# Optimization experiments

Hardware: AMD Instinct MI355X
Metric: run time of the kernel (lower is better)

## Reference

```python
import jax, jax.numpy as jnp
import numpy as np

N, E, D, L = 50000, 600000, 128, 2  # nodes, edges, hidden_dim, num_gnn_layers
NEG_SLOPE = 0.2  # PyG GATv2Conv default negative_slope


def setup_inputs() -> dict:
    key = jax.random.key(0)
    ks = jax.random.split(key, 10)
    s = 1.0 / np.sqrt(D)
    return {
        "x": jax.random.normal(ks[0], (N, D), jnp.float32),
        "edge_index": jax.random.randint(ks[1], (2, E), 0, N, dtype=jnp.int32),
        # per-layer GATv2 params (stacked over L layers)
        "Wl": jax.random.normal(ks[2], (L, D, D), jnp.float32) * s,  # lin_l (source)
        "bl": jnp.zeros((L, D), jnp.float32),
        "Wr": jax.random.normal(ks[3], (L, D, D), jnp.float32) * s,  # lin_r (target)
        "br": jnp.zeros((L, D), jnp.float32),
        "att": jax.random.normal(ks[4], (L, D), jnp.float32) * s,
        "bias": jnp.zeros((L, D), jnp.float32),
        # shared residual Linear
        "W_res": jax.random.normal(ks[5], (D, D), jnp.float32) * s,
        "b_res": jnp.zeros((D,), jnp.float32),
    }


def reference(x, edge_index, Wl, bl, Wr, br, att, bias, W_res, b_res):
    n = x.shape[0]
    # add self loops (PyG GATv2Conv default add_self_loops=True)
    loops = jnp.arange(n, dtype=edge_index.dtype)
    src = jnp.concatenate([edge_index[0], loops])  # source j (messages)
    dst = jnp.concatenate([edge_index[1], loops])  # target i (aggregation)

    def conv(h, i):
        xl = h @ Wl[i] + bl[i]  # [N, D] source transform
        xr = h @ Wr[i] + br[i]  # [N, D] target transform
        m = xl[src] + xr[dst]   # [E+N, D] gathered edge messages
        e = jnp.einsum('ed,d->e', jnp.where(m > 0, m, NEG_SLOPE * m), att[i])
        # segment softmax over incoming edges of each destination node
        emax = jax.lax.stop_gradient(jax.ops.segment_max(e, dst, num_segments=n))
        ex = jnp.exp(e - emax[dst])
        denom = jax.ops.segment_sum(ex, dst, num_segments=n)
        alpha = ex / (denom[dst] + 1e-16)
        out = jax.ops.segment_sum(alpha[:, None] * xl[src], dst, num_segments=n)
        return out + bias[i]

    for i in range(Wl.shape[0]):
        x = jax.nn.relu(conv(x, i) + x @ W_res + b_res)
    return x
```

## Files before the change

### kernel.cpp

```cpp
#include <hip/hip_runtime.h>
#include <math.h>


#define DIM 128
#define NEG_SLOPE 0.2f
#define TPW 4

typedef __attribute__((ext_vector_type(8))) short short8;
typedef __attribute__((ext_vector_type(4))) float floatx4;

static __device__ __forceinline__ unsigned short f2b(float f) {
    unsigned u = __float_as_uint(f);
    unsigned r = (u + 0x7FFFu + ((u >> 16) & 1u)) >> 16;
    return (unsigned short)r;
}
static __device__ __forceinline__ float b2f(unsigned short h) {
    return __uint_as_float(((unsigned)h) << 16);
}

__global__ void k_init_counts(int* __restrict__ counts, int n) {
    int i = blockIdx.x * blockDim.x + threadIdx.x;
    if (i < n) counts[i] = 1;
}

__global__ void k_count(const int* __restrict__ dst, int E, int* __restrict__ counts) {
    int k = blockIdx.x * blockDim.x + threadIdx.x;
    if (k < E) atomicAdd(&counts[dst[k]], 1);
}

__global__ void k_scan1(const int* __restrict__ counts, int n,
                        int* __restrict__ rowptr, int* __restrict__ bsum) {
    __shared__ int s[256];
    int tid = threadIdx.x;
    int i = blockIdx.x * 256 + tid;
    int v = (i < n) ? counts[i] : 0;
    s[tid] = v;
    __syncthreads();
    for (int off = 1; off < 256; off <<= 1) {
        int t = (tid >= off) ? s[tid - off] : 0;
        __syncthreads();
        s[tid] += t;
        __syncthreads();
    }
    if (i < n) rowptr[i + 1] = s[tid];
    if (tid == 255) bsum[blockIdx.x] = s[255];
}

__global__ void k_scan2(int* __restrict__ bsum, int nb) {
    __shared__ int s[256];
    int tid = threadIdx.x;
    int v = (tid < nb) ? bsum[tid] : 0;
    s[tid] = v;
    __syncthreads();
    for (int off = 1; off < 256; off <<= 1) {
        int t = (tid >= off) ? s[tid - off] : 0;
        __syncthreads();
        s[tid] += t;
        __syncthreads();
    }
    if (tid < nb) bsum[tid] = s[tid];
}

__global__ void k_scan3(int* __restrict__ rowptr, const int* __restrict__ bsum,
                        int n, int* __restrict__ counts_to_cursors) {
    int i = blockIdx.x * 256 + threadIdx.x;
    if (i < n) {
        int add = (blockIdx.x > 0) ? bsum[blockIdx.x - 1] : 0;
        int cnt = counts_to_cursors[i];
        int v = rowptr[i + 1] + add;
        rowptr[i + 1] = v;
        counts_to_cursors[i] = v - cnt;
    }
    if (i == 0) rowptr[0] = 0;
}

__global__ void k_scatter(const int* __restrict__ src, const int* __restrict__ dst,
                          int E, int n, int* __restrict__ cur, int* __restrict__ srt) {
    int k = blockIdx.x * blockDim.x + threadIdx.x;
    int tot = E + n;
    if (k >= tot) return;
    int s, d;
    if (k < E) { s = src[k]; d = dst[k]; }
    else       { s = k - E;  d = s; }
    int p = atomicAdd(&cur[d], 1);
    srt[p] = s;
}

__global__ void k_wfrag(const float* __restrict__ Wl, const float* __restrict__ Wr,
                        const float* __restrict__ Wres, unsigned short* __restrict__ out) {
    int idx = blockIdx.x * blockDim.x + threadIdx.x;
    if (idx >= 2 * 3 * 4 * 8 * 64) return;
    int lane = idx & 63;
    int nr   = (idx >> 6) & 7;
    int ks   = (idx >> 9) & 3;
    int v    = idx >> 11;
    int sec = v % 3, l = v / 3;
    const float* W = (sec == 0) ? (Wl + l * DIM * DIM)
                   : (sec == 1) ? (Wr + l * DIM * DIM) : Wres;
    int nn = nr * 16 + (lane & 15);
    int k0 = ks * 32 + ((lane >> 4) << 3);
    ushort4 a, b;
    a.x = f2b(W[(k0 + 0) * DIM + nn]); a.y = f2b(W[(k0 + 1) * DIM + nn]);
    a.z = f2b(W[(k0 + 2) * DIM + nn]); a.w = f2b(W[(k0 + 3) * DIM + nn]);
    b.x = f2b(W[(k0 + 4) * DIM + nn]); b.y = f2b(W[(k0 + 5) * DIM + nn]);
    b.z = f2b(W[(k0 + 6) * DIM + nn]); b.w = f2b(W[(k0 + 7) * DIM + nn]);
    *(ushort4*)(out + (size_t)idx * 8) = a;
    *(ushort4*)(out + (size_t)idx * 8 + 4) = b;
}

__global__ void k_hfrag(const float* __restrict__ h, unsigned short* __restrict__ out,
                        int n, int ntiles) {
    int idx = blockIdx.x * blockDim.x + threadIdx.x;
    if (idx >= ntiles * 256) return;
    int lane = idx & 63;
    int ks   = (idx >> 6) & 3;
    int tile = idx >> 8;
    int row  = tile * 16 + (lane & 15);
    int col0 = ks * 32 + ((lane >> 4) << 3);
    ushort4 a = {0, 0, 0, 0}, b = {0, 0, 0, 0};
    if (row < n) {
        float4 v0 = *(const float4*)(h + (size_t)row * DIM + col0);
        float4 v1 = *(const float4*)(h + (size_t)row * DIM + col0 + 4);
        a.x = f2b(v0.x); a.y = f2b(v0.y); a.z = f2b(v0.z); a.w = f2b(v0.w);
        b.x = f2b(v1.x); b.y = f2b(v1.y); b.z = f2b(v1.z); b.w = f2b(v1.w);
    }
    *(ushort4*)(out + (size_t)idx * 8) = a;
    *(ushort4*)(out + (size_t)idx * 8 + 4) = b;
}

__global__ __launch_bounds__(256, 2) void k_gemm(
    const unsigned short* __restrict__ hfrag, const unsigned short* __restrict__ wfrag,
    const float* __restrict__ bl, const float* __restrict__ br, const float* __restrict__ bres,
    unsigned short* __restrict__ XLb, float* __restrict__ XR, float* __restrict__ RES,
    int ntiles)
{
    int sec  = blockIdx.y;
    int lane = threadIdx.x & 63;
    int w    = threadIdx.x >> 6;

    const unsigned short* wbase = wfrag + (size_t)sec * (4 * 8 * 64 * 8);
    short8 bf[4][8];
#pragma unroll
    for (int ks = 0; ks < 4; ks++)
#pragma unroll
        for (int nr = 0; nr < 8; nr++)
            bf[ks][nr] = *(const short8*)(wbase + (((ks * 8 + nr) * 64 + lane) << 3));

    const float* bias = (sec == 0) ? bl : (sec == 1) ? br : bres;
    int colb = (lane >> 4) << 2;
    float4 bv[8];
#pragma unroll
    for (int nr = 0; nr < 8; nr++) bv[nr] = *(const float4*)(bias + nr * 16 + colb);

    int wid = blockIdx.x * 4 + w;
#pragma unroll
    for (int i = 0; i < TPW; i++) {
        int t = wid * TPW + i;
        if (t >= ntiles) break;
        short8 a[4];
#pragma unroll
        for (int ks = 0; ks < 4; ks++)
            a[ks] = *(const short8*)(hfrag + (((t * 4 + ks) * 64 + lane) << 3));
        floatx4 acc[8];
#pragma unroll
        for (int nr = 0; nr < 8; nr++) acc[nr] = (floatx4){0.f, 0.f, 0.f, 0.f};
#pragma unroll
        for (int ks = 0; ks < 4; ks++)
#pragma unroll
            for (int nr = 0; nr < 8; nr++)
                acc[nr] = __builtin_amdgcn_mfma_f32_16x16x32_bf16(bf[ks][nr], a[ks], acc[nr], 0, 0, 0);

        int row = t * 16 + (lane & 15);
        size_t rb = (size_t)row * DIM;
#pragma unroll
        for (int nr = 0; nr < 8; nr++) {
            float4 o;
            o.x = acc[nr][0] + bv[nr].x;
            o.y = acc[nr][1] + bv[nr].y;
            o.z = acc[nr][2] + bv[nr].z;
            o.w = acc[nr][3] + bv[nr].w;
            int col = nr * 16 + colb;
            if (sec == 0) {
                ushort4 u;
                u.x = f2b(o.x); u.y = f2b(o.y); u.z = f2b(o.z); u.w = f2b(o.w);
                *(ushort4*)(XLb + rb + col) = u;
            } else if (sec == 1) {
                *(float4*)(XR + rb + col) = o;
            } else {
                *(float4*)(RES + rb + col) = o;
            }
        }
    }
}

__global__ __launch_bounds__(256) void k_aggr(
    const unsigned short* __restrict__ XLb, const float* __restrict__ XR,
    const float* __restrict__ RES, const float* __restrict__ att,
    const float* __restrict__ bias, const int* __restrict__ rowptr,
    const int* __restrict__ srt, float* __restrict__ outF,
    unsigned short* __restrict__ fragOut, int writeFrag, int n)
{
    int wave = threadIdx.x >> 6;
    int lane = threadIdx.x & 63;
    int node = blockIdx.x * 4 + wave;
    if (node >= n) return;
    int half = lane >> 5, sl = lane & 31;
    int d0 = sl << 2;

    float4 a4 = *(const float4*)(att + d0);
    float4 x4 = *(const float4*)(XR + (size_t)node * DIM + d0);
    int beg = rowptr[node], end = rowptr[node + 1];
    int len = end - beg;
    int hl = (len + 1) >> 1;
    int sb = beg + half * hl;
    int se = half ? end : (beg + hl);

    float m = -INFINITY, den = 0.f;
    float ax = 0.f, ay = 0.f, az = 0.f, aw = 0.f;

    int j = sb;
    for (; j + 4 <= se; j += 4) {
        int s0 = srt[j], s1 = srt[j + 1], s2 = srt[j + 2], s3 = srt[j + 3];
        ushort4 u0 = *(const ushort4*)(XLb + (size_t)s0 * DIM + d0);
        ushort4 u1 = *(const ushort4*)(XLb + (size_t)s1 * DIM + d0);
        ushort4 u2 = *(const ushort4*)(XLb + (size_t)s2 * DIM + d0);
        ushort4 u3 = *(const ushort4*)(XLb + (size_t)s3 * DIM + d0);
        float v0x = b2f(u0.x), v0y = b2f(u0.y), v0z = b2f(u0.z), v0w = b2f(u0.w);
        float v1x = b2f(u1.x), v1y = b2f(u1.y), v1z = b2f(u1.z), v1w = b2f(u1.w);
        float v2x = b2f(u2.x), v2y = b2f(u2.y), v2z = b2f(u2.z), v2w = b2f(u2.w);
        float v3x = b2f(u3.x), v3y = b2f(u3.y), v3z = b2f(u3.z), v3w = b2f(u3.w);
        float t, p0, p1, p2, p3;
        t = v0x + x4.x; p0  = fmaxf(t, NEG_SLOPE * t) * a4.x;
        t = v0y + x4.y; p0 += fmaxf(t, NEG_SLOPE * t) * a4.y;
        t = v0z + x4.z; p0 += fmaxf(t, NEG_SLOPE * t) * a4.z;
        t = v0w + x4.w; p0 += fmaxf(t, NEG_SLOPE * t) * a4.w;
        t = v1x + x4.x; p1  = fmaxf(t, NEG_SLOPE * t) * a4.x;
        t = v1y + x4.y; p1 += fmaxf(t, NEG_SLOPE * t) * a4.y;
        t = v1z + x4.z; p1 += fmaxf(t, NEG_SLOPE * t) * a4.z;
        t = v1w + x4.w; p1 += fmaxf(t, NEG_SLOPE * t) * a4.w;
        t = v2x + x4.x; p2  = fmaxf(t, NEG_SLOPE * t) * a4.x;
        t = v2y + x4.y; p2 += fmaxf(t, NEG_SLOPE * t) * a4.y;
        t = v2z + x4.z; p2 += fmaxf(t, NEG_SLOPE * t) * a4.z;
        t = v2w + x4.w; p2 += fmaxf(t, NEG_SLOPE * t) * a4.w;
        t = v3x + x4.x; p3  = fmaxf(t, NEG_SLOPE * t) * a4.x;
        t = v3y + x4.y; p3 += fmaxf(t, NEG_SLOPE * t) * a4.y;
        t = v3z + x4.z; p3 += fmaxf(t, NEG_SLOPE * t) * a4.z;
        t = v3w + x4.w; p3 += fmaxf(t, NEG_SLOPE * t) * a4.w;
#pragma unroll
        for (int off = 16; off >= 1; off >>= 1) {
            p0 += __shfl_xor(p0, off);
            p1 += __shfl_xor(p1, off);
            p2 += __shfl_xor(p2, off);
            p3 += __shfl_xor(p3, off);
        }
        float pm = fmaxf(fmaxf(p0, p1), fmaxf(p2, p3));
        float mn = fmaxf(m, pm);
        float c  = __expf(m - mn);
        float w0 = __expf(p0 - mn), w1 = __expf(p1 - mn);
        float w2 = __expf(p2 - mn), w3 = __expf(p3 - mn);
        ax = ax * c + w0 * v0x + w1 * v1x + w2 * v2x + w3 * v3x;
        ay = ay * c + w0 * v0y + w1 * v1y + w2 * v2y + w3 * v3y;
        az = az * c + w0 * v0z + w1 * v1z + w2 * v2z + w3 * v3z;
        aw = aw * c + w0 * v0w + w1 * v1w + w2 * v2w + w3 * v3w;
        den = den * c + w0 + w1 + w2 + w3;
        m = mn;
    }
    for (; j < se; j++) {
        int s0 = srt[j];
        ushort4 u0 = *(const ushort4*)(XLb + (size_t)s0 * DIM + d0);
        float v0x = b2f(u0.x), v0y = b2f(u0.y), v0z = b2f(u0.z), v0w = b2f(u0.w);
        float t, p0;
        t = v0x + x4.x; p0  = fmaxf(t, NEG_SLOPE * t) * a4.x;
        t = v0y + x4.y; p0 += fmaxf(t, NEG_SLOPE * t) * a4.y;
        t = v0z + x4.z; p0 += fmaxf(t, NEG_SLOPE * t) * a4.z;
        t = v0w + x4.w; p0 += fmaxf(t, NEG_SLOPE * t) * a4.w;
#pragma unroll
        for (int off = 16; off >= 1; off >>= 1) p0 += __shfl_xor(p0, off);
        float mn = fmaxf(m, p0);
        float c  = __expf(m - mn);
        float w0 = __expf(p0 - mn);
        ax = ax * c + w0 * v0x;
        ay = ay * c + w0 * v0y;
        az = az * c + w0 * v0z;
        aw = aw * c + w0 * v0w;
        den = den * c + w0;
        m = mn;
    }

    float om   = __shfl_xor(m, 32);
    float oden = __shfl_xor(den, 32);
    float ox = __shfl_xor(ax, 32), oy = __shfl_xor(ay, 32);
    float oz = __shfl_xor(az, 32), ow = __shfl_xor(aw, 32);
    float M  = fmaxf(m, om);
    float se_ = __expf(m - M), so = __expf(om - M);
    float D  = den * se_ + oden * so + 1e-16f;
    float inv = 1.f / D;

    float4 r4 = *(const float4*)(RES + (size_t)node * DIM + d0);
    float4 b4 = *(const float4*)(bias + d0);
    float4 o;
    o.x = fmaxf((ax * se_ + ox * so) * inv + b4.x + r4.x, 0.f);
    o.y = fmaxf((ay * se_ + oy * so) * inv + b4.y + r4.y, 0.f);
    o.z = fmaxf((az * se_ + oz * so) * inv + b4.z + r4.z, 0.f);
    o.w = fmaxf((aw * se_ + ow * so) * inv + b4.w + r4.w, 0.f);

    if (half == 0) {
        if (writeFrag) {
            int tile = node >> 4;
            int ks = sl >> 3;
            int li = (node & 15) + (((sl >> 1) & 3) << 4);
            int j0 = (sl & 1) << 2;
            ushort4 u;
            u.x = f2b(o.x); u.y = f2b(o.y); u.z = f2b(o.z); u.w = f2b(o.w);
            *(ushort4*)(fragOut + ((size_t)((tile * 4 + ks) * 64 + li) << 3) + j0) = u;
        } else {
            *(float4*)(outF + (size_t)node * DIM + d0) = o;
        }
    }
}

extern "C" void kernel_launch(void* const* d_in, const int* in_sizes, int n_in,
                              void* d_out, int out_size, void* d_ws, size_t ws_size,
                              hipStream_t stream) {
    const float* x    = (const float*)d_in[0];
    const int*   ei   = (const int*)d_in[1];
    const float* Wl   = (const float*)d_in[2];
    const float* bl   = (const float*)d_in[3];
    const float* Wr   = (const float*)d_in[4];
    const float* br   = (const float*)d_in[5];
    const float* att  = (const float*)d_in[6];
    const float* bias = (const float*)d_in[7];
    const float* Wres = (const float*)d_in[8];
    const float* bres = (const float*)d_in[9];

    int n = in_sizes[0] / DIM;
    int E = in_sizes[1] / 2;
    int ntiles = (n + 15) >> 4;
    const int* srcIdx = ei;
    const int* dstIdx = ei + E;

    float* xr   = (float*)d_ws;
    float* resb = xr + (size_t)n * DIM;
    unsigned short* xlb   = (unsigned short*)(resb + (size_t)n * DIM);
    unsigned short* hfrag = xlb + (size_t)n * DIM;
    unsigned short* wfrag = hfrag + (size_t)ntiles * 16 * DIM;
    int* rowptr = (int*)(wfrag + 2 * 3 * DIM * DIM);
    int* tmpc   = rowptr + (n + 1);
    int* srt    = tmpc + n;
    int* bsum   = srt + (E + n);

    int nb1 = (n + 255) / 256;

    k_init_counts<<<(n + 255) / 256, 256, 0, stream>>>(tmpc, n);
    k_count<<<(E + 255) / 256, 256, 0, stream>>>(dstIdx, E, tmpc);
    k_scan1<<<nb1, 256, 0, stream>>>(tmpc, n, rowptr, bsum);
    k_scan2<<<1, 256, 0, stream>>>(bsum, nb1);
    k_scan3<<<nb1, 256, 0, stream>>>(rowptr, bsum, n, tmpc);
    k_scatter<<<(E + n + 255) / 256, 256, 0, stream>>>(srcIdx, dstIdx, E, n, tmpc, srt);
    k_wfrag<<<(2 * 3 * 4 * 8 * 64 + 255) / 256, 256, 0, stream>>>(Wl, Wr, Wres, wfrag);
    k_hfrag<<<(ntiles * 256 + 255) / 256, 256, 0, stream>>>(x, hfrag, n, ntiles);

    int gx = (ntiles + 4 * TPW - 1) / (4 * TPW);
    for (int l = 0; l < 2; l++) {
        dim3 g(gx, 3);
        k_gemm<<<g, 256, 0, stream>>>(hfrag, wfrag + (size_t)l * 3 * 4 * 8 * 64 * 8,
                                      bl + (size_t)l * DIM, br + (size_t)l * DIM, bres,
                                      xlb, xr, resb, ntiles);
        k_aggr<<<(n + 3) / 4, 256, 0, stream>>>(xlb, xr, resb, att + (size_t)l * DIM,
                                                bias + (size_t)l * DIM, rowptr, srt,
                                                (float*)d_out, hfrag, (l == 0) ? 1 : 0, n);
    }
}
```

Before: 218.7 us.

## Merge preprocessing kernels, single-block scan, bf16 XR, 8-way packed aggregation

Replaces the three-kernel scan with a single 1024-thread block scan, zero-initialises counts with a memset, and fuses weight and feature fragment conversion into one launch. XR is stored as bf16 to halve its traffic. The aggregation loop processes 8 edges per iteration using packed f32 ops and a rewritten leaky-ReLU (0.6t+0.4|t|), with masked tails. Risks include unaligned int4 index loads, over-reads past segment ends, and extra bf16 rounding of XR.

New measurement: 354.7 us. 62.2% more time.

```diff
diff --git a/kernel.cpp b/kernel.cpp
--- a/kernel.cpp
+++ b/kernel.cpp
@@ -8,6 +8,7 @@
 
 typedef __attribute__((ext_vector_type(8))) short short8;
 typedef __attribute__((ext_vector_type(4))) float floatx4;
+typedef __attribute__((ext_vector_type(2))) float f32x2;
 
 static __device__ __forceinline__ unsigned short f2b(float f) {
     unsigned u = __float_as_uint(f);
@@ -17,10 +18,32 @@
 static __device__ __forceinline__ float b2f(unsigned short h) {
     return __uint_as_float(((unsigned)h) << 16);
 }
-
-__global__ void k_init_counts(int* __restrict__ counts, int n) {
-    int i = blockIdx.x * blockDim.x + threadIdx.x;
-    if (i < n) counts[i] = 1;
+static __device__ __forceinline__ f32x2 cvt2(unsigned u) {
+    f32x2 r;
+    r.x = __uint_as_float(u << 16);
+    r.y = __uint_as_float(u & 0xffff0000u);
+    return r;
+}
+static __device__ __forceinline__ f32x2 pk_add(f32x2 a, f32x2 b) {
+    f32x2 d;
+    asm("v_pk_add_f32 %0, %1, %2" : "=v"(d) : "v"(a), "v"(b));
+    return d;
+}
+static __device__ __forceinline__ f32x2 pk_mul(f32x2 a, f32x2 b) {
+    f32x2 d;
+    asm("v_pk_mul_f32 %0, %1, %2" : "=v"(d) : "v"(a), "v"(b));
+    return d;
+}
+static __device__ __forceinline__ f32x2 pk_fma(f32x2 a, f32x2 b, f32x2 c) {
+    f32x2 d;
+    asm("v_pk_fma_f32 %0, %1, %2, %3" : "=v"(d) : "v"(a), "v"(b), "v"(c));
+    return d;
+}
+static __device__ __forceinline__ f32x2 pk_abs2(f32x2 a) {
+    f32x2 r;
+    r.x = __builtin_fabsf(a.x);
+    r.y = __builtin_fabsf(a.y);
+    return r;
 }
 
 __global__ void k_count(const int* __restrict__ dst, int E, int* __restrict__ counts) {
@@ -28,50 +51,31 @@
     if (k < E) atomicAdd(&counts[dst[k]], 1);
 }
 
-__global__ void k_scan1(const int* __restrict__ counts, int n,
-                        int* __restrict__ rowptr, int* __restrict__ bsum) {
-    __shared__ int s[256];
+__global__ __launch_bounds__(1024) void k_scan(int* __restrict__ cnt, int n,
+                                               int* __restrict__ rowptr) {
+    __shared__ int sh[1024];
     int tid = threadIdx.x;
-    int i = blockIdx.x * 256 + tid;
-    int v = (i < n) ? counts[i] : 0;
-    s[tid] = v;
+    int chunk = (n + 1023) >> 10;
+    int b = tid * chunk;
+    int e = min(b + chunk, n);
+    int s = 0;
+    for (int i = b; i < e; i++) s += cnt[i] + 1;
+    sh[tid] = s;
     __syncthreads();
-    for (int off = 1; off < 256; off <<= 1) {
-        int t = (tid >= off) ? s[tid - off] : 0;
+    for (int off = 1; off < 1024; off <<= 1) {
+        int t = (tid >= off) ? sh[tid - off] : 0;
         __syncthreads();
-        s[tid] += t;
+        sh[tid] += t;
         __syncthreads();
     }
-    if (i < n) rowptr[i + 1] = s[tid];
-    if (tid == 255) bsum[blockIdx.x] = s[255];
-}
-
-__global__ void k_scan2(int* __restrict__ bsum, int nb) {
-    __shared__ int s[256];
-    int tid = threadIdx.x;
-    int v = (tid < nb) ? bsum[tid] : 0;
-    s[tid] = v;
-    __syncthreads();
-    for (int off = 1; off < 256; off <<= 1) {
-        int t = (tid >= off) ? s[tid - off] : 0;
-        __syncthreads();
-        s[tid] += t;
-        __syncthreads();
-    }
-    if (tid < nb) bsum[tid] = s[tid];
-}
-
-__global__ void k_scan3(int* __restrict__ rowptr, const int* __restrict__ bsum,
-                        int n, int* __restrict__ counts_to_cursors) {
-    int i = blockIdx.x * 256 + threadIdx.x;
-    if (i < n) {
-        int add = (blockIdx.x > 0) ? bsum[blockIdx.x - 1] : 0;
-        int cnt = counts_to_cursors[i];
-        int v = rowptr[i + 1] + add;
-        rowptr[i + 1] = v;
-        counts_to_cursors[i] = v - cnt;
-    }
-    if (i == 0) rowptr[0] = 0;
+    int run = sh[tid] - s;
+    for (int i = b; i < e; i++) {
+        int c = cnt[i] + 1;
+        cnt[i] = run;
+        run += c;
+        rowptr[i + 1] = run;
+    }
+    if (tid == 0) rowptr[0] = 0;
 }
 
 __global__ void k_scatter(const int* __restrict__ src, const int* __restrict__ dst,
@@ -86,53 +90,54 @@
     srt[p] = s;
 }
 
-__global__ void k_wfrag(const float* __restrict__ Wl, const float* __restrict__ Wr,
-                        const float* __restrict__ Wres, unsigned short* __restrict__ out) {
-    int idx = blockIdx.x * blockDim.x + threadIdx.x;
-    if (idx >= 2 * 3 * 4 * 8 * 64) return;
-    int lane = idx & 63;
-    int nr   = (idx >> 6) & 7;
-    int ks   = (idx >> 9) & 3;
-    int v    = idx >> 11;
-    int sec = v % 3, l = v / 3;
-    const float* W = (sec == 0) ? (Wl + l * DIM * DIM)
-                   : (sec == 1) ? (Wr + l * DIM * DIM) : Wres;
-    int nn = nr * 16 + (lane & 15);
-    int k0 = ks * 32 + ((lane >> 4) << 3);
-    ushort4 a, b;
-    a.x = f2b(W[(k0 + 0) * DIM + nn]); a.y = f2b(W[(k0 + 1) * DIM + nn]);
-    a.z = f2b(W[(k0 + 2) * DIM + nn]); a.w = f2b(W[(k0 + 3) * DIM + nn]);
-    b.x = f2b(W[(k0 + 4) * DIM + nn]); b.y = f2b(W[(k0 + 5) * DIM + nn]);
-    b.z = f2b(W[(k0 + 6) * DIM + nn]); b.w = f2b(W[(k0 + 7) * DIM + nn]);
-    *(ushort4*)(out + (size_t)idx * 8) = a;
-    *(ushort4*)(out + (size_t)idx * 8 + 4) = b;
-}
-
-__global__ void k_hfrag(const float* __restrict__ h, unsigned short* __restrict__ out,
-                        int n, int ntiles) {
-    int idx = blockIdx.x * blockDim.x + threadIdx.x;
-    if (idx >= ntiles * 256) return;
-    int lane = idx & 63;
-    int ks   = (idx >> 6) & 3;
-    int tile = idx >> 8;
-    int row  = tile * 16 + (lane & 15);
-    int col0 = ks * 32 + ((lane >> 4) << 3);
-    ushort4 a = {0, 0, 0, 0}, b = {0, 0, 0, 0};
-    if (row < n) {
-        float4 v0 = *(const float4*)(h + (size_t)row * DIM + col0);
-        float4 v1 = *(const float4*)(h + (size_t)row * DIM + col0 + 4);
-        a.x = f2b(v0.x); a.y = f2b(v0.y); a.z = f2b(v0.z); a.w = f2b(v0.w);
-        b.x = f2b(v1.x); b.y = f2b(v1.y); b.z = f2b(v1.z); b.w = f2b(v1.w);
-    }
-    *(ushort4*)(out + (size_t)idx * 8) = a;
-    *(ushort4*)(out + (size_t)idx * 8 + 4) = b;
+__global__ void k_pre(const float* __restrict__ Wl, const float* __restrict__ Wr,
+                      const float* __restrict__ Wres, unsigned short* __restrict__ wfrag,
+                      const float* __restrict__ h, unsigned short* __restrict__ hfrag,
+                      int n, int ntiles) {
+    int blk = blockIdx.x;
+    if (blk < 48) {
+        int idx = blk * 256 + threadIdx.x;
+        int lane = idx & 63;
+        int nr   = (idx >> 6) & 7;
+        int ks   = (idx >> 9) & 3;
+        int v    = idx >> 11;
+        int sec = v % 3, l = v / 3;
+        const float* W = (sec == 0) ? (Wl + l * DIM * DIM)
+                       : (sec == 1) ? (Wr + l * DIM * DIM) : Wres;
+        int nn = nr * 16 + (lane & 15);
+        int k0 = ks * 32 + ((lane >> 4) << 3);
+        ushort4 a, b;
+        a.x = f2b(W[(k0 + 0) * DIM + nn]); a.y = f2b(W[(k0 + 1) * DIM + nn]);
+        a.z = f2b(W[(k0 + 2) * DIM + nn]); a.w = f2b(W[(k0 + 3) * DIM + nn]);
+        b.x = f2b(W[(k0 + 4) * DIM + nn]); b.y = f2b(W[(k0 + 5) * DIM + nn]);
+        b.z = f2b(W[(k0 + 6) * DIM + nn]); b.w = f2b(W[(k0 + 7) * DIM + nn]);
+        *(ushort4*)(wfrag + (size_t)idx * 8) = a;
+        *(ushort4*)(wfrag + (size_t)idx * 8 + 4) = b;
+    } else {
+        int idx = (blk - 48) * 256 + threadIdx.x;
+        if (idx >= ntiles * 256) return;
+        int lane = idx & 63;
+        int ks   = (idx >> 6) & 3;
+        int tile = idx >> 8;
+        int row  = tile * 16 + (lane & 15);
+        int col0 = ks * 32 + ((lane >> 4) << 3);
+        ushort4 a = {0, 0, 0, 0}, b = {0, 0, 0, 0};
+        if (row < n) {
+            float4 v0 = *(const float4*)(h + (size_t)row * DIM + col0);
+            float4 v1 = *(const float4*)(h + (size_t)row * DIM + col0 + 4);
+            a.x = f2b(v0.x); a.y = f2b(v0.y); a.z = f2b(v0.z); a.w = f2b(v0.w);
+            b.x = f2b(v1.x); b.y = f2b(v1.y); b.z = f2b(v1.z); b.w = f2b(v1.w);
+        }
+        *(ushort4*)(hfrag + (size_t)idx * 8) = a;
+        *(ushort4*)(hfrag + (size_t)idx * 8 + 4) = b;
+    }
 }
 
 __global__ __launch_bounds__(256, 2) void k_gemm(
     const unsigned short* __restrict__ hfrag, const unsigned short* __restrict__ wfrag,
     const float* __restrict__ bl, const float* __restrict__ br, const float* __restrict__ bres,
-    unsigned short* __restrict__ XLb, float* __restrict__ XR, float* __restrict__ RES,
-    int ntiles)
+    unsigned short* __restrict__ XLb, unsigned short* __restrict__ XRb,
+    float* __restrict__ RES, int ntiles)
 {
     int sec  = blockIdx.y;
     int lane = threadIdx.x & 63;
@@ -180,21 +185,31 @@
             o.z = acc[nr][2] + bv[nr].z;
             o.w = acc[nr][3] + bv[nr].w;
             int col = nr * 16 + colb;
-            if (sec == 0) {
+            if (sec == 2) {
+                *(float4*)(RES + rb + col) = o;
+            } else {
                 ushort4 u;
                 u.x = f2b(o.x); u.y = f2b(o.y); u.z = f2b(o.z); u.w = f2b(o.w);
-                *(ushort4*)(XLb + rb + col) = u;
-            } else if (sec == 1) {
-                *(float4*)(XR + rb + col) = o;
-            } else {
-                *(float4*)(RES + rb + col) = o;
+                if (sec == 0) *(ushort4*)(XLb + rb + col) = u;
+                else          *(ushort4*)(XRb + rb + col) = u;
             }
         }
     }
 }
 
+#define EDGE_LOGIT(K, JOFF)                                              \
+    f32x2 v01_##K = cvt2(e##K.x), v23_##K = cvt2(e##K.y);                \
+    f32x2 t01_##K = pk_add(v01_##K, x01);                                \
+    f32x2 t23_##K = pk_add(v23_##K, x23);                                \
+    f32x2 pp_##K = pk_mul(a6_01, t01_##K);                               \
+    pp_##K = pk_fma(a4_01, pk_abs2(t01_##K), pp_##K);                    \
+    pp_##K = pk_fma(a6_23, t23_##K, pp_##K);                             \
+    pp_##K = pk_fma(a4_23, pk_abs2(t23_##K), pp_##K);                    \
+    float p##K = pp_##K.x + pp_##K.y;                                    \
+    p##K = (j + JOFF < se) ? p##K : -3.0e38f;
+
 __global__ __launch_bounds__(256) void k_aggr(
-    const unsigned short* __restrict__ XLb, const float* __restrict__ XR,
+    const unsigned short* __restrict__ XLb, const unsigned short* __restrict__ XRb,
     const float* __restrict__ RES, const float* __restrict__ att,
     const float* __restrict__ bias, const int* __restrict__ rowptr,
     const int* __restrict__ srt, float* __restrict__ outF,
@@ -207,83 +222,69 @@
     int half = lane >> 5, sl = lane & 31;
     int d0 = sl << 2;
 
-    float4 a4 = *(const float4*)(att + d0);
-    float4 x4 = *(const float4*)(XR + (size_t)node * DIM + d0);
+    float a0 = att[d0], a1 = att[d0 + 1], a2 = att[d0 + 2], a3 = att[d0 + 3];
+    f32x2 a6_01 = {0.6f * a0, 0.6f * a1}, a6_23 = {0.6f * a2, 0.6f * a3};
+    f32x2 a4_01 = {0.4f * a0, 0.4f * a1}, a4_23 = {0.4f * a2, 0.4f * a3};
+
+    uint2 xru = *(const uint2*)(XRb + (size_t)node * DIM + d0);
+    f32x2 x01 = cvt2(xru.x), x23 = cvt2(xru.y);
+
     int beg = rowptr[node], end = rowptr[node + 1];
     int len = end - beg;
     int hl = (len + 1) >> 1;
     int sb = beg + half * hl;
     int se = half ? end : (beg + hl);
 
+    const uint2* R = (const uint2*)XLb;
+
     float m = -INFINITY, den = 0.f;
     float ax = 0.f, ay = 0.f, az = 0.f, aw = 0.f;
 
-    int j = sb;
-    for (; j + 4 <= se; j += 4) {
-        int s0 = srt[j], s1 = srt[j + 1], s2 = srt[j + 2], s3 = srt[j + 3];
-        ushort4 u0 = *(const ushort4*)(XLb + (size_t)s0 * DIM + d0);
-        ushort4 u1 = *(const ushort4*)(XLb + (size_t)s1 * DIM + d0);
-        ushort4 u2 = *(const ushort4*)(XLb + (size_t)s2 * DIM + d0);
-        ushort4 u3 = *(const ushort4*)(XLb + (size_t)s3 * DIM + d0);
-        float v0x = b2f(u0.x), v0y = b2f(u0.y), v0z = b2f(u0.z), v0w = b2f(u0.w);
-        float v1x = b2f(u1.x), v1y = b2f(u1.y), v1z = b2f(u1.z), v1w = b2f(u1.w);
-        float v2x = b2f(u2.x), v2y = b2f(u2.y), v2z = b2f(u2.z), v2w = b2f(u2.w);
-        float v3x = b2f(u3.x), v3y = b2f(u3.y), v3z = b2f(u3.z), v3w = b2f(u3.w);
-        float t, p0, p1, p2, p3;
-        t = v0x + x4.x; p0  = fmaxf(t, NEG_SLOPE * t) * a4.x;
-        t = v0y + x4.y; p0 += fmaxf(t, NEG_SLOPE * t) * a4.y;
-        t = v0z + x4.z; p0 += fmaxf(t, NEG_SLOPE * t) * a4.z;
-        t = v0w + x4.w; p0 += fmaxf(t, NEG_SLOPE * t) * a4.w;
-        t = v1x + x4.x; p1  = fmaxf(t, NEG_SLOPE * t) * a4.x;
-        t = v1y + x4.y; p1 += fmaxf(t, NEG_SLOPE * t) * a4.y;
-        t = v1z + x4.z; p1 += fmaxf(t, NEG_SLOPE * t) * a4.z;
-        t = v1w + x4.w; p1 += fmaxf(t, NEG_SLOPE * t) * a4.w;
-        t = v2x + x4.x; p2  = fmaxf(t, NEG_SLOPE * t) * a4.x;
-        t = v2y + x4.y; p2 += fmaxf(t, NEG_SLOPE * t) * a4.y;
-        t = v2z + x4.z; p2 += fmaxf(t, NEG_SLOPE * t) * a4.z;
-        t = v2w + x4.w; p2 += fmaxf(t, NEG_SLOPE * t) * a4.w;
-        t = v3x + x4.x; p3  = fmaxf(t, NEG_SLOPE * t) * a4.x;
-        t = v3y + x4.y; p3 += fmaxf(t, NEG_SLOPE * t) * a4.y;
-        t = v3z + x4.z; p3 += fmaxf(t, NEG_SLOPE * t) * a4.z;
-        t = v3w + x4.w; p3 += fmaxf(t, NEG_SLOPE * t) * a4.w;
+    for (int j = sb; j < se; j += 8) {
+        int4 sA = *(const int4*)(srt + j);
+        int4 sB = *(const int4*)(srt + j + 4);
+        int i0 = sA.x;
+        int i1 = (j + 1 < se) ? sA.y : i0;
+        int i2 = (j + 2 < se) ? sA.z : i0;
+        int i3 = (j + 3 < se) ? sA.w : i0;
+        int i4 = (j + 4 < se) ? sB.x : i0;
+        int i5 = (j + 5 < se) ? sB.y : i0;
+        int i6 = (j + 6 < se) ? sB.z : i0;
+        int i7 = (j + 7 < se) ? sB.w : i0;
+        uint2 e0 = R[(size_t)i0 * 32 + sl];
+        uint2 e1 = R[(size_t)i1 * 32 + sl];
+        uint2 e2 = R[(size_t)i2 * 32 + sl];
+        uint2 e3 = R[(size_t)i3 * 32 + sl];
+        uint2 e4 = R[(size_t)i4 * 32 + sl];
+        uint2 e5 = R[(size_t)i5 * 32 + sl];
+        uint2 e6 = R[(size_t)i6 * 32 + sl];
+        uint2 e7 = R[(size_t)i7 * 32 + sl];
+        EDGE_LOGIT(0, 0) EDGE_LOGIT(1, 1) EDGE_LOGIT(2, 2) EDGE_LOGIT(3, 3)
+        EDGE_LOGIT(4, 4) EDGE_LOGIT(5, 5) EDGE_LOGIT(6, 6) EDGE_LOGIT(7, 7)
 #pragma unroll
         for (int off = 16; off >= 1; off >>= 1) {
-            p0 += __shfl_xor(p0, off);
-            p1 += __shfl_xor(p1, off);
-            p2 += __shfl_xor(p2, off);
-            p3 += __shfl_xor(p3, off);
+            p0 += __shfl_xor(p0, off); p1 += __shfl_xor(p1, off);
+            p2 += __shfl_xor(p2, off); p3 += __shfl_xor(p3, off);
+            p4 += __shfl_xor(p4, off); p5 += __shfl_xor(p5, off);
+            p6 += __shfl_xor(p6, off); p7 += __shfl_xor(p7, off);
         }
-        float pm = fmaxf(fmaxf(p0, p1), fmaxf(p2, p3));
+        float pm = fmaxf(fmaxf(fmaxf(p0, p1), fmaxf(p2, p3)),
+                         fmaxf(fmaxf(p4, p5), fmaxf(p6, p7)));
         float mn = fmaxf(m, pm);
         float c  = __expf(m - mn);
         float w0 = __expf(p0 - mn), w1 = __expf(p1 - mn);
         float w2 = __expf(p2 - mn), w3 = __expf(p3 - mn);
-        ax = ax * c + w0 * v0x + w1 * v1x + w2 * v2x + w3 * v3x;
-        ay = ay * c + w0 * v0y + w1 * v1y + w2 * v2y + w3 * v3y;
-        az = az * c + w0 * v0z + w1 * v1z + w2 * v2z + w3 * v3z;
-        aw = aw * c + w0 * v0w + w1 * v1w + w2 * v2w + w3 * v3w;
-        den = den * c + w0 + w1 + w2 + w3;
-        m = mn;
-    }
-    for (; j < se; j++) {
-        int s0 = srt[j];
-        ushort4 u0 = *(const ushort4*)(XLb + (size_t)s0 * DIM + d0);
-        float v0x = b2f(u0.x), v0y = b2f(u0.y), v0z = b2f(u0.z), v0w = b2f(u0.w);
-        float t, p0;
-        t = v0x + x4.x; p0  = fmaxf(t, NEG_SLOPE * t) * a4.x;
-        t = v0y + x4.y; p0 += fmaxf(t, NEG_SLOPE * t) * a4.y;
-        t = v0z + x4.z; p0 += fmaxf(t, NEG_SLOPE * t) * a4.z;
-        t = v0w + x4.w; p0 += fmaxf(t, NEG_SLOPE * t) * a4.w;
-#pragma unroll
-        for (int off = 16; off >= 1; off >>= 1) p0 += __shfl_xor(p0, off);
-        float mn = fmaxf(m, p0);
-        float c  = __expf(m - mn);
-        float w0 = __expf(p0 - mn);
-        ax = ax * c + w0 * v0x;
-        ay = ay * c + w0 * v0y;
-        az = az * c + w0 * v0z;
-        aw = aw * c + w0 * v0w;
-        den = den * c + w0;
+        float w4 = __expf(p4 - mn), w5 = __expf(p5 - mn);
+        float w6 = __expf(p6 - mn), w7 = __expf(p7 - mn);
+        ax = ax * c + w0 * v01_0.x + w1 * v01_1.x + w2 * v01_2.x + w3 * v01_3.x
+                    + w4 * v01_4.x + w5 * v01_5.x + w6 * v01_6.x + w7 * v01_7.x;
+        ay = ay * c + w0 * v01_0.y + w1 * v01_1.y + w2 * v01_2.y + w3 * v01_3.y
+                    + w4 * v01_4.y + w5 * v01_5.y + w6 * v01_6.y + w7 * v01_7.y;
+        az = az * c + w0 * v23_0.x + w1 * v23_1.x + w2 * v23_2.x + w3 * v23_3.x
+                    + w4 * v23_4.x + w5 * v23_5.x + w6 * v23_6.x + w7 * v23_7.x;
+        aw = aw * c + w0 * v23_0.y + w1 * v23_1.y + w2 * v23_2.y + w3 * v23_3.y
+                    + w4 * v23_4.y + w5 * v23_5.y + w6 * v23_6.y + w7 * v23_7.y;
+        den = den * c + (((w0 + w1) + (w2 + w3)) + ((w4 + w5) + (w6 + w7)));
         m = mn;
     }
 
@@ -339,34 +340,28 @@
     const int* srcIdx = ei;
     const int* dstIdx = ei + E;
 
-    float* xr   = (float*)d_ws;
-    float* resb = xr + (size_t)n * DIM;
+    float* resb = (float*)d_ws;
     unsigned short* xlb   = (unsigned short*)(resb + (size_t)n * DIM);
-    unsigned short* hfrag = xlb + (size_t)n * DIM;
+    unsigned short* xrb   = xlb + (size_t)n * DIM;
+    unsigned short* hfrag = xrb + (size_t)n * DIM;
     unsigned short* wfrag = hfrag + (size_t)ntiles * 16 * DIM;
     int* rowptr = (int*)(wfrag + 2 * 3 * DIM * DIM);
     int* tmpc   = rowptr + (n + 1);
     int* srt    = tmpc + n;
-    int* bsum   = srt + (E + n);
-
-    int nb1 = (n + 255) / 256;
-
-    k_init_counts<<<(n + 255) / 256, 256, 0, stream>>>(tmpc, n);
+
+    hipMemsetAsync(tmpc, 0, (size_t)n * sizeof(int), stream);
     k_count<<<(E + 255) / 256, 256, 0, stream>>>(dstIdx, E, tmpc);
-    k_scan1<<<nb1, 256, 0, stream>>>(tmpc, n, rowptr, bsum);
-    k_scan2<<<1, 256, 0, stream>>>(bsum, nb1);
-    k_scan3<<<nb1, 256, 0, stream>>>(rowptr, bsum, n, tmpc);
+    k_pre<<<48 + ntiles, 256, 0, stream>>>(Wl, Wr, Wres, wfrag, x, hfrag, n, ntiles);
+    k_scan<<<1, 1024, 0, stream>>>(tmpc, n, rowptr);
     k_scatter<<<(E + n + 255) / 256, 256, 0, stream>>>(srcIdx, dstIdx, E, n, tmpc, srt);
-    k_wfrag<<<(2 * 3 * 4 * 8 * 64 + 255) / 256, 256, 0, stream>>>(Wl, Wr, Wres, wfrag);
-    k_hfrag<<<(ntiles * 256 + 255) / 256, 256, 0, stream>>>(x, hfrag, n, ntiles);
 
     int gx = (ntiles + 4 * TPW - 1) / (4 * TPW);
     for (int l = 0; l < 2; l++) {
         dim3 g(gx, 3);
         k_gemm<<<g, 256, 0, stream>>>(hfrag, wfrag + (size_t)l * 3 * 4 * 8 * 64 * 8,
                                       bl + (size_t)l * DIM, br + (size_t)l * DIM, bres,
-                                      xlb, xr, resb, ntiles);
-        k_aggr<<<(n + 3) / 4, 256, 0, stream>>>(xlb, xr, resb, att + (size_t)l * DIM,
+                                      xlb, xrb, resb, ntiles);
+        k_aggr<<<(n + 3) / 4, 256, 0, stream>>>(xlb, xrb, resb, att + (size_t)l * DIM,
                                                 bias + (size_t)l * DIM, rowptr, srt,
                                                 (float*)d_out, hfrag, (l == 0) ? 1 : 0, n);
     }
```
